# Kernel optimization log

Measured on AMD Instinct MI355X. Metric: run time of the kernel, lower is better.

The kernel has to match this reference:

```python
import jax, jax.numpy as jnp
from jax import lax
import numpy as np

B, T, U, V = 4, 300, 64, 1024
FEAT, H, L = 80, 512, 3            # encoder: 3-layer bidirectional LSTM
HD = 512                           # decoder hidden (1 layer)
ENC_OUT = DEC_OUT = 512
INNER = 512
DMAX = max(FEAT, 2 * H)            # padded input dim for stacked encoder weights
NEG = -1e30


def setup_inputs() -> dict:
    key = jax.random.key(0)
    ks = jax.random.split(key, 20)
    s = 1.0 / np.sqrt(H)
    u = lambda k, shp: jax.random.uniform(k, shp, jnp.float32, -s, s)
    inputs = jax.random.normal(ks[0], (B, T, FEAT), jnp.float32)
    inputs_length = jax.random.randint(ks[1], (B,), T // 2, T + 1, jnp.int32)
    targets = jax.random.randint(ks[2], (B, U), 1, V, jnp.int32)
    targets_length = jax.random.randint(ks[3], (B,), U // 2, U + 1, jnp.int32)
    enc_Wih = u(ks[4], (L, 2, 4 * H, DMAX))   # layer0 uses first FEAT cols
    enc_Whh = u(ks[5], (L, 2, 4 * H, H))
    enc_b = u(ks[6], (L, 2, 4 * H))           # b_ih + b_hh fused
    enc_proj_W = u(ks[7], (ENC_OUT, 2 * H))
    enc_proj_b = u(ks[8], (ENC_OUT,))
    dec_emb = u(ks[9], (V, HD)).at[0].set(0.0)  # padding_idx=0
    dec_Wih = u(ks[10], (4 * HD, HD))
    dec_Whh = u(ks[11], (4 * HD, HD))
    dec_b = u(ks[12], (4 * HD,))
    dec_proj_W = u(ks[13], (DEC_OUT, HD))
    dec_proj_b = u(ks[14], (DEC_OUT,))
    j_fwd_W = u(ks[15], (INNER, ENC_OUT + DEC_OUT))
    j_fwd_b = u(ks[16], (INNER,))
    j_proj_W = u(ks[17], (V, INNER))
    j_proj_b = u(ks[18], (V,))
    return dict(inputs=inputs, inputs_length=inputs_length, targets=targets,
                targets_length=targets_length, enc_Wih=enc_Wih, enc_Whh=enc_Whh,
                enc_b=enc_b, enc_proj_W=enc_proj_W, enc_proj_b=enc_proj_b,
                dec_emb=dec_emb, dec_Wih=dec_Wih, dec_Whh=dec_Whh, dec_b=dec_b,
                dec_proj_W=dec_proj_W, dec_proj_b=dec_proj_b, j_fwd_W=j_fwd_W,
                j_fwd_b=j_fwd_b, j_proj_W=j_proj_W, j_proj_b=j_proj_b)


def lstm_layer(x, Wih, Whh, b):
    # x: [B, T, Din]; torch gate order (i, f, g, o)
    Bb = x.shape[0]
    Hh = Whh.shape[1]
    xg = jnp.einsum('btd,gd->btg', x, Wih) + b  # precompute input projections

    def step(carry, xt):
        h, c = carry
        g = xt + h @ Whh.T
        i, f, gg, o = jnp.split(g, 4, axis=-1)
        c = jax.nn.sigmoid(f) * c + jax.nn.sigmoid(i) * jnp.tanh(gg)
        h = jax.nn.sigmoid(o) * jnp.tanh(c)
        return (h, c), h

    z = jnp.zeros((Bb, Hh), x.dtype)
    _, hs = lax.scan(step, (z, z), xg.transpose(1, 0, 2))
    return hs.transpose(1, 0, 2)


def reverse_padded(x, lengths):
    # reverse each sequence within its valid length (packed-sequence semantics)
    t = jnp.arange(x.shape[1])
    idx = jnp.where(t[None] < lengths[:, None], lengths[:, None] - 1 - t[None], t[None])
    return jnp.take_along_axis(x, idx[:, :, None], axis=1)


def rnnt_loss(log_probs, targets, T_len, U_len):
    # log_probs: [B, T, U+1, V], blank = 0
    Bb, Tt, U1, _ = log_probs.shape
    Uu = U1 - 1
    blank = log_probs[..., 0]                                   # [B,T,U+1]
    idx = jnp.broadcast_to(targets[:, None, :, None], (Bb, Tt, Uu, 1))
    lab = jnp.take_along_axis(log_probs[:, :, :Uu, :], idx, axis=3)[..., 0]  # [B,T,U]

    def row_update(a, c):
        # solves x[u] = logaddexp(a[u], x[u-1] + c[u-1]) via log-space cumsum
        C = jnp.concatenate([jnp.zeros((Bb, 1), a.dtype), jnp.cumsum(c, axis=1)], axis=1)
        return C + lax.cumlogsumexp(a - C, axis=1)

    a0 = jnp.full((Bb, U1), NEG, log_probs.dtype).at[:, 0].set(0.0)
    alpha0 = row_update(a0, lab[:, 0])

    def step(alpha_prev, xs):
        bl_prev, lab_t = xs
        alpha = row_update(alpha_prev + bl_prev, lab_t)
        return alpha, alpha

    xs = (blank[:, :-1].transpose(1, 0, 2), lab[:, 1:].transpose(1, 0, 2))
    _, alphas = lax.scan(step, alpha0, xs)                      # [T-1,B,U+1]
    alphas = jnp.concatenate([alpha0[None], alphas], axis=0)    # [T,B,U+1]
    b_idx = jnp.arange(Bb)
    ll = alphas[T_len - 1, b_idx, U_len] + blank[b_idx, T_len - 1, U_len]
    return -jnp.mean(ll)


def reference(inputs, inputs_length, targets, targets_length, enc_Wih, enc_Whh,
              enc_b, enc_proj_W, enc_proj_b, dec_emb, dec_Wih, dec_Whh, dec_b,
              dec_proj_W, dec_proj_b, j_fwd_W, j_fwd_b, j_proj_W, j_proj_b):
    # ---- encoder: stacked bi-LSTM + projection ----
    mask = (jnp.arange(T)[None] < inputs_length[:, None])[..., None].astype(inputs.dtype)
    x = inputs
    for l in range(L):
        Din = x.shape[-1]
        fwd = lstm_layer(x, enc_Wih[l, 0, :, :Din], enc_Whh[l, 0], enc_b[l, 0])
        bwd = reverse_padded(
            lstm_layer(reverse_padded(x, inputs_length), enc_Wih[l, 1, :, :Din],
                       enc_Whh[l, 1], enc_b[l, 1]), inputs_length)
        x = jnp.concatenate([fwd, bwd], axis=-1) * mask
    enc = jnp.einsum('bth,oh->bto', x, enc_proj_W) + enc_proj_b  # [B,T,ENC_OUT]

    # ---- decoder: blank-prepended targets -> embed -> LSTM -> projection ----
    dec_in = jnp.pad(targets, ((0, 0), (1, 0)))                  # [B,U+1]
    demb = dec_emb[dec_in]
    dmask = (jnp.arange(U + 1)[None] < (targets_length + 1)[:, None])[..., None].astype(demb.dtype)
    dh = lstm_layer(demb, dec_Wih, dec_Whh, dec_b) * dmask
    dec = jnp.einsum('buh,oh->buo', dh, dec_proj_W) + dec_proj_b  # [B,U+1,DEC_OUT]

    # ---- joint: broadcast T x (U+1), split concat-matmul into two matmuls ----
    We, Wd = j_fwd_W[:, :ENC_OUT], j_fwd_W[:, ENC_OUT:]
    hj = jnp.tanh(jnp.einsum('bto,io->bti', enc, We)[:, :, None, :]
                  + jnp.einsum('buo,io->bui', dec, Wd)[:, None, :, :] + j_fwd_b)
    logits = jnp.einsum('btui,vi->btuv', hj, j_proj_W) + j_proj_b  # [B,T,U+1,V]
    log_probs = jax.nn.log_softmax(logits, axis=-1)

    return rnnt_loss(log_probs, targets, inputs_length, targets_length)
```

## Files before the change

kernel.cpp:

```cpp
#include <hip/hip_runtime.h>
#include <hip/hip_bf16.h>

#define B_ 4
#define T_ 300
#define U_ 64
#define U1_ 65
#define V_ 1024
#define H_ 512
#define G4_ 2048
#define NW_ 32
#define RPB_ (T_ * U1_)
#define NTILE_ 305
#define RPAD_ 19520

typedef __hip_bfloat16 bf16;
typedef unsigned long long u64;
typedef __attribute__((ext_vector_type(8))) short short8;
typedef __attribute__((ext_vector_type(4))) float floatx4;

__device__ __forceinline__ float b2f(bf16 x) { return __bfloat162float(x); }
__device__ __forceinline__ bf16 f2b(float x) { return __float2bfloat16(x); }
__device__ __forceinline__ short bf16bits(float x) {
  bf16 h = __float2bfloat16(x);
  return *reinterpret_cast<short*>(&h);
}
__device__ __forceinline__ short8 pack8(float4 a, float4 b) {
  short8 p;
  p[0] = bf16bits(a.x); p[1] = bf16bits(a.y); p[2] = bf16bits(a.z); p[3] = bf16bits(a.w);
  p[4] = bf16bits(b.x); p[5] = bf16bits(b.y); p[6] = bf16bits(b.z); p[7] = bf16bits(b.w);
  return p;
}
__device__ __forceinline__ float sigm_(float x) { return 1.f / (1.f + __expf(-x)); }
__device__ __forceinline__ float tanh_(float x) { return 1.f - 2.f / (1.f + __expf(2.f * x)); }
__device__ __forceinline__ float lae_(float x, float y) {
  float m = fmaxf(x, y);
  float n = fminf(x, y);
  return m + __logf(1.f + __expf(n - m));
}

__global__ void zero_hpk_kernel(u64* __restrict__ a) {
  int i = blockIdx.x * 256 + threadIdx.x;
  if (i < 7 * 4096) a[i] = 0ull;
}

__global__ void prep_kernel(const float* __restrict__ in, bf16* __restrict__ x0) {
  int i = blockIdx.x * 256 + threadIdx.x;
  if (i < B_ * T_ * 128) {
    int k = i & 127;
    int row = i >> 7;
    float v = (k < 80) ? in[row * 80 + k] : 0.f;
    x0[(size_t)row * 1024 + k] = f2b(v);
  }
}

__global__ void embed_kernel(const float* __restrict__ emb, const int* __restrict__ tgt,
                             bf16* __restrict__ demb) {
  int i = blockIdx.x * 256 + threadIdx.x;
  if (i >= B_ * U1_ * 512) return;
  int k = i & 511;
  int bu = i >> 9;
  int u = bu % U1_, b = bu / U1_;
  int id = (u == 0) ? 0 : tgt[b * U_ + u - 1];
  demb[i] = f2b(emb[(size_t)id * 512 + k]);
}

__global__ __launch_bounds__(256) void gemm_kernel(
    const bf16* __restrict__ A, int lda,
    const float* __restrict__ W, int ldw,
    const float* __restrict__ bias,
    void* __restrict__ Cout, int out_f32, int ldc,
    int M, int K) {
  __shared__ __align__(16) bf16 As[64][72];
  __shared__ __align__(16) bf16 Bs[64][72];
  int m0 = blockIdx.x * 64, n0 = blockIdx.y * 64;
  int tid = threadIdx.x, w = tid >> 6, l = tid & 63;
  int l4 = l & 15, lq = l >> 4;
  floatx4 acc[4];
#pragma unroll
  for (int nt = 0; nt < 4; ++nt) acc[nt] = (floatx4){0.f, 0.f, 0.f, 0.f};
  for (int k0 = 0; k0 < K; k0 += 64) {
    __syncthreads();
#pragma unroll
    for (int q = 0; q < 2; ++q) {
      int cc = tid + q * 256;
      int r = cc >> 3, kc = (cc & 7) * 8;
      short8 va = {0, 0, 0, 0, 0, 0, 0, 0};
      int gm = m0 + r;
      if (gm < M) va = *(const short8*)(A + (size_t)gm * lda + k0 + kc);
      *(short8*)(&As[r][kc]) = va;
      const float* wp = W + (size_t)(n0 + r) * ldw + k0 + kc;
      float4 w0 = *(const float4*)(wp);
      float4 w1 = *(const float4*)(wp + 4);
      *(short8*)(&Bs[r][kc]) = pack8(w0, w1);
    }
    __syncthreads();
#pragma unroll
    for (int kk = 0; kk < 64; kk += 32) {
      short8 a = *(const short8*)(&As[w * 16 + l4][kk + lq * 8]);
#pragma unroll
      for (int nt = 0; nt < 4; ++nt) {
        short8 bb = *(const short8*)(&Bs[nt * 16 + l4][kk + lq * 8]);
        acc[nt] = __builtin_amdgcn_mfma_f32_16x16x32_bf16(a, bb, acc[nt], 0, 0, 0);
      }
    }
  }
#pragma unroll
  for (int nt = 0; nt < 4; ++nt) {
    int col = n0 + nt * 16 + l4;
    float bv = bias ? bias[col] : 0.f;
#pragma unroll
    for (int r = 0; r < 4; ++r) {
      int row = m0 + w * 16 + lq * 4 + r;
      if (row < M) {
        float v = acc[nt][r] + bv;
        if (out_f32) ((float*)Cout)[(size_t)row * ldc + col] = v;
        else ((bf16*)Cout)[(size_t)row * ldc + col] = f2b(v);
      }
    }
  }
}

__global__ __launch_bounds__(256, 1) void scan_kernel(
    const float* __restrict__ xg,
    const float* __restrict__ whh,
    const int* __restrict__ len_raw, int len_add,
    int Tmax, int bwd_mask,
    bf16* __restrict__ out, int out_stride,
    int dec_d,
    const float* __restrict__ xg2, const float* __restrict__ whh2,
    const int* __restrict__ len_raw2, int len_add2,
    int Tmax2, bf16* __restrict__ out2, int out_stride2,
    u64* __restrict__ hpk) {
  int w = blockIdx.x, d = blockIdx.y;
  int tid = threadIdx.x;
  bool isdec = (d == dec_d);
  const float* xg_d = isdec ? xg2 : xg + (size_t)d * B_ * Tmax * G4_;
  const float* whh_d = isdec ? whh2 : whh + (size_t)d * G4_ * H_;
  const int* lens = isdec ? len_raw2 : len_raw;
  int ladd = isdec ? len_add2 : len_add;
  int tmax = isdec ? Tmax2 : Tmax;
  bf16* outp = isdec ? out2 : out;
  int ostride = isdec ? out_stride2 : out_stride;
  int ocol = isdec ? 0 : d * H_;
  bool bwd = isdec ? false : ((bwd_mask >> d) & 1);
  u64* hp = hpk + (size_t)d * 4096;

  int sub = tid >> 6;
  int l = tid & 63;
  int col = l & 15;
  int lq = l >> 4;
  int gate = col & 3;
  int dloc = col >> 2;
  int dim = w * 16 + sub * 4 + dloc;
  int grow = gate * H_ + dim;
  int sb = l & 12;

  __shared__ int len_s[4];
  __shared__ __align__(16) bf16 h_lds[2][16][512];

  if (tid < 4) len_s[tid] = lens[tid] + ladd;
  {
    unsigned* hz = (unsigned*)&h_lds[0][0][0];
#pragma unroll
    for (int i = 0; i < 32; ++i) hz[tid + i * 256] = 0u;
  }

  short8 bfr[16];
  {
    const float* wp = whh_d + (size_t)grow * H_ + lq * 8;
#pragma unroll
    for (int ks2 = 0; ks2 < 16; ++ks2) {
      float4 w0 = *(const float4*)(wp + ks2 * 32);
      float4 w1 = *(const float4*)(wp + ks2 * 32 + 4);
      bfr[ks2] = pack8(w0, w1);
    }
  }
  __syncthreads();
  int smax = max(max(len_s[0], len_s[1]), max(len_s[2], len_s[3]));

  int D0 = sub * 128 + 2 * l;
  float cst = 0.f;
  char* hbase = (char*)&h_lds[0][0][0];
  unsigned rsw = (unsigned)((l & 7) << 4);
  unsigned rbyte = (unsigned)((l & 15) * 1024 + lq * 16);

  float xv[4];
  if (l < 16) {
#pragma unroll
    for (int b = 0; b < 4; ++b) {
      int lb = len_s[b];
      int rt = bwd ? (lb - 1) : 0;
      xv[b] = xg_d[((size_t)b * tmax + rt) * G4_ + grow];
    }
  }

  for (int s = 0; s < smax; ++s) {
    int p = s & 1;
    char* pl = hbase + p * 16384;
    if (s == 0) {
    } else {
      const u64* src = hp + ((s - 1) & 1) * 2048;
      u64 v[8];
      for (;;) {
        bool ok = true;
#pragma unroll
        for (int b = 0; b < 4; ++b) {
          v[2 * b] = __hip_atomic_load(src + b * 512 + D0, __ATOMIC_RELAXED,
                                       __HIP_MEMORY_SCOPE_AGENT);
          v[2 * b + 1] = __hip_atomic_load(src + b * 512 + D0 + 1, __ATOMIC_RELAXED,
                                           __HIP_MEMORY_SCOPE_AGENT);
          ok &= ((int)(unsigned)v[2 * b] == s) & ((int)(unsigned)v[2 * b + 1] == s);
        }
        if (__all(ok)) break;
      }
      unsigned cb = (unsigned)(D0 * 2);
#pragma unroll
      for (int b = 0; b < 4; ++b) {
        float f0 = __uint_as_float((unsigned)(v[2 * b] >> 32));
        float f1 = __uint_as_float((unsigned)(v[2 * b + 1] >> 32));
        bf16 h0 = f2b(f0), h1 = f2b(f1);
        float r0 = f0 - b2f(h0), r1 = f1 - b2f(h1);
        bf16 e0 = f2b(r0), e1 = f2b(r1);
        unsigned hi = (unsigned)*(unsigned short*)&h0 |
                      ((unsigned)*(unsigned short*)&h1 << 16);
        unsigned lo = (unsigned)*(unsigned short*)&e0 |
                      ((unsigned)*(unsigned short*)&e1 << 16);
        *(unsigned*)(pl + (((unsigned)(b * 1024) + cb) ^ (unsigned)(b << 4))) = hi;
        *(unsigned*)(pl + (((unsigned)((b + 4) * 1024) + cb) ^ (unsigned)((b + 4) << 4))) = lo;
      }
    }
    __syncthreads();
    float xvn[4];
    if (l < 16) {
      int sn = s + 1;
#pragma unroll
      for (int b = 0; b < 4; ++b) {
        int lb = len_s[b];
        int rt = bwd ? (lb - 1 - sn) : sn;
        if (sn >= lb) rt = 0;
        xvn[b] = xg_d[((size_t)b * tmax + rt) * G4_ + grow];
      }
    }
    floatx4 accA = (floatx4){0.f, 0.f, 0.f, 0.f};
    floatx4 accB = (floatx4){0.f, 0.f, 0.f, 0.f};
#pragma unroll
    for (int k2 = 0; k2 < 16; k2 += 2) {
      short8 a0 = *(const short8*)(pl + ((rbyte + (unsigned)(k2 * 64)) ^ rsw));
      short8 a1 = *(const short8*)(pl + ((rbyte + (unsigned)((k2 + 1) * 64)) ^ rsw));
      accA = __builtin_amdgcn_mfma_f32_16x16x32_bf16(a0, bfr[k2], accA, 0, 0, 0);
      accB = __builtin_amdgcn_mfma_f32_16x16x32_bf16(a1, bfr[k2 + 1], accB, 0, 0, 0);
    }
    floatx4 acc = accA + accB;
    float hout = 0.f;
#pragma unroll
    for (int r = 0; r < 4; ++r) {
      float v2 = acc[r] + __shfl(acc[r], col + 16, 64);
      if (l < 16) v2 += xv[r];
      float gi = __shfl(v2, sb + 0, 64);
      float gf = __shfl(v2, sb + 1, 64);
      float gg = __shfl(v2, sb + 2, 64);
      float go = __shfl(v2, sb + 3, 64);
      if (l < 16 && (l & 3) == r && s < len_s[r]) {
        cst = sigm_(gf) * cst + sigm_(gi) * tanh_(gg);
        hout = sigm_(go) * tanh_(cst);
      }
    }
    if (l < 16) {
      int b = l & 3;
      u64 pkt = ((u64)__float_as_uint(hout) << 32) | (unsigned)(s + 1);
      __hip_atomic_store(hp + p * 2048 + b * 512 + dim, pkt,
                         __ATOMIC_RELAXED, __HIP_MEMORY_SCOPE_AGENT);
      if (s < len_s[b]) {
        int t = bwd ? (len_s[b] - 1 - s) : s;
        outp[((size_t)b * tmax + t) * ostride + ocol + dim] = f2b(hout);
      }
    }
#pragma unroll
    for (int b = 0; b < 4; ++b) xv[b] = xvn[b];
  }
}

__global__ __launch_bounds__(256) void joint_kernel(
    const float* __restrict__ ea, const float* __restrict__ da,
    const float* __restrict__ Wp, const float* __restrict__ pb,
    const int* __restrict__ targets,
    float* __restrict__ blankraw, float* __restrict__ labraw,
    float* __restrict__ jstats) {
  __shared__ __align__(16) bf16 As[64][72];
  __shared__ __align__(16) bf16 Bs[256][72];
  __shared__ float bias_s[256];
  __shared__ int tgt_s[64];
  __shared__ float pstat[64][2][2];

  int tid = threadIdx.x;
  int tile = blockIdx.x, cb = blockIdx.y, b = blockIdx.z;
  int r0 = tile * 64;

  bias_s[tid & 255] = pb[cb * 256 + (tid & 255)];
  if (tid < 64) {
    int r = r0 + tid;
    int u = r % U1_;
    tgt_s[tid] = (r < RPB_ && u < U_) ? targets[b * U_ + u] : -1;
  }
  int si = tid >> 2;
  int sseg = (tid & 3) * 16;
  int sr = r0 + si;
  bool svalid = sr < RPB_;
  int st = svalid ? sr / U1_ : 0;
  int su = svalid ? sr % U1_ : 0;
  const float* ep = ea + ((size_t)(b * T_ + st)) * 512 + sseg;
  const float* dp = da + ((size_t)(b * U1_ + su)) * 512 + sseg;

  int wid = tid >> 6, l = tid & 63;
  int wm = wid >> 1, wn = wid & 1;
  int l4 = l & 15, lq = l >> 4;

  floatx4 acc[2][8];
#pragma unroll
  for (int ms = 0; ms < 2; ++ms)
#pragma unroll
    for (int nt = 0; nt < 8; ++nt) acc[ms][nt] = (floatx4){0.f, 0.f, 0.f, 0.f};

  for (int k0 = 0; k0 < 512; k0 += 64) {
    __syncthreads();
    {
      const float* e = ep + k0;
      const float* d = dp + k0;
#pragma unroll
      for (int h = 0; h < 2; ++h) {
        float4 e0 = *(const float4*)(e + h * 8);
        float4 e1 = *(const float4*)(e + h * 8 + 4);
        float4 d0 = *(const float4*)(d + h * 8);
        float4 d1 = *(const float4*)(d + h * 8 + 4);
        short8 pk = {0, 0, 0, 0, 0, 0, 0, 0};
        if (svalid) {
          pk[0] = bf16bits(tanh_(e0.x + d0.x));
          pk[1] = bf16bits(tanh_(e0.y + d0.y));
          pk[2] = bf16bits(tanh_(e0.z + d0.z));
          pk[3] = bf16bits(tanh_(e0.w + d0.w));
          pk[4] = bf16bits(tanh_(e1.x + d1.x));
          pk[5] = bf16bits(tanh_(e1.y + d1.y));
          pk[6] = bf16bits(tanh_(e1.z + d1.z));
          pk[7] = bf16bits(tanh_(e1.w + d1.w));
        }
        *(short8*)(&As[si][sseg + h * 8]) = pk;
      }
    }
#pragma unroll
    for (int q = 0; q < 8; ++q) {
      int cc = tid + q * 256;
      int r = cc >> 3, kc = (cc & 7) * 8;
      const float* wp = Wp + (size_t)(cb * 256 + r) * 512 + k0 + kc;
      float4 w0 = *(const float4*)(wp);
      float4 w1 = *(const float4*)(wp + 4);
      *(short8*)(&Bs[r][kc]) = pack8(w0, w1);
    }
    __syncthreads();
#pragma unroll
    for (int kk = 0; kk < 64; kk += 32) {
      short8 af[2], bf8[8];
#pragma unroll
      for (int ms = 0; ms < 2; ++ms)
        af[ms] = *(const short8*)(&As[wm * 32 + ms * 16 + l4][kk + lq * 8]);
#pragma unroll
      for (int nt = 0; nt < 8; ++nt)
        bf8[nt] = *(const short8*)(&Bs[wn * 128 + nt * 16 + l4][kk + lq * 8]);
#pragma unroll
      for (int ms = 0; ms < 2; ++ms)
#pragma unroll
        for (int nt = 0; nt < 8; ++nt)
          acc[ms][nt] = __builtin_amdgcn_mfma_f32_16x16x32_bf16(af[ms], bf8[nt], acc[ms][nt], 0, 0, 0);
    }
  }
#pragma unroll
  for (int ms = 0; ms < 2; ++ms) {
#pragma unroll
    for (int r = 0; r < 4; ++r) {
      int i = wm * 32 + ms * 16 + lq * 4 + r;
      int grow = r0 + i;
      bool valid = grow < RPB_;
      int tg = tgt_s[i];
      float v[8];
      float mx = -1e30f;
#pragma unroll
      for (int nt = 0; nt < 8; ++nt) {
        int colc = wn * 128 + nt * 16 + l4;
        float x = acc[ms][nt][r] + bias_s[colc];
        v[nt] = x;
        mx = fmaxf(mx, x);
        int gcol = cb * 256 + colc;
        if (valid) {
          if (gcol == 0) blankraw[(size_t)b * RPB_ + grow] = x;
          if (gcol == tg) labraw[(size_t)b * RPB_ + grow] = x;
        }
      }
#pragma unroll
      for (int dd = 1; dd < 16; dd <<= 1) mx = fmaxf(mx, __shfl_xor(mx, dd, 64));
      float se = 0.f;
#pragma unroll
      for (int nt = 0; nt < 8; ++nt) se += __expf(v[nt] - mx);
#pragma unroll
      for (int dd = 1; dd < 16; dd <<= 1) se += __shfl_xor(se, dd, 64);
      if (l4 == 0) { pstat[i][wn][0] = mx; pstat[i][wn][1] = se; }
    }
  }
  __syncthreads();
  if (tid < 64) {
    float ma = pstat[tid][0][0], sa = pstat[tid][0][1];
    float mb = pstat[tid][1][0], sb = pstat[tid][1][1];
    float mc = fmaxf(ma, mb);
    float sc = sa * __expf(ma - mc) + sb * __expf(mb - mc);
    size_t o = (((size_t)b * RPAD_ + r0 + tid) * 4 + cb) * 2;
    jstats[o] = mc;
    jstats[o + 1] = sc;
  }
}

__global__ void finalize_kernel(const float* __restrict__ jstats,
                                float* __restrict__ blank, float* __restrict__ lab) {
  int g = blockIdx.x * 256 + threadIdx.x;
  if (g >= B_ * RPB_) return;
  int b = g / RPB_, r = g % RPB_;
  const float* st = jstats + ((size_t)b * RPAD_ + r) * 8;
  float M = fmaxf(fmaxf(st[0], st[2]), fmaxf(st[4], st[6]));
  float s = st[1] * __expf(st[0] - M) + st[3] * __expf(st[2] - M) +
            st[5] * __expf(st[4] - M) + st[7] * __expf(st[6] - M);
  float lse = M + __logf(s);
  blank[g] -= lse;
  if ((r % U1_) < U_) lab[g] -= lse;
}

__global__ void loss_kernel(const float* __restrict__ blank, const float* __restrict__ lab,
                            const int* __restrict__ Tl, const int* __restrict__ Ul,
                            float* __restrict__ outp) {
  int b = threadIdx.x >> 6;
  int l = threadIdx.x & 63;
  int TL = Tl[b], UL = Ul[b];
  float alpha_l = 0.f, alpha0 = 0.f;
  for (int t = 0; t < TL; ++t) {
    float a_u0, a_l1;
    if (t == 0) { a_u0 = 0.f; a_l1 = -1e30f; }
    else {
      const float* bl = blank + ((size_t)b * T_ + (t - 1)) * U1_;
      a_u0 = alpha0 + bl[0];
      a_l1 = alpha_l + bl[l + 1];
    }
    const float* lb = lab + ((size_t)b * T_ + t) * U1_;
    float C = lb[l];
#pragma unroll
    for (int dd = 1; dd < 64; dd <<= 1) {
      float o = __shfl_up(C, dd, 64);
      if (l >= dd) C += o;
    }
    float S = a_l1 - C;
#pragma unroll
    for (int dd = 1; dd < 64; dd <<= 1) {
      float o = __shfl_up(S, dd, 64);
      if (l >= dd) S = lae_(S, o);
    }
    alpha_l = C + lae_(a_u0, S);
    alpha0 = a_u0;
  }
  float av = (UL == 0) ? alpha0 : __shfl(alpha_l, UL - 1, 64);
  float ll = av + blank[((size_t)b * T_ + (TL - 1)) * U1_ + UL];
  __shared__ float lls[4];
  if (l == 0) lls[b] = ll;
  __syncthreads();
  if (threadIdx.x == 0) outp[0] = -0.25f * (lls[0] + lls[1] + lls[2] + lls[3]);
}

static constexpr size_t OFF_XG = 0;
static constexpr size_t OFF_XA = OFF_XG + (size_t)2 * B_ * T_ * G4_ * 4;
static constexpr size_t OFF_XB = OFF_XA + (size_t)B_ * T_ * 1024 * 2;
static constexpr size_t OFF_ENC = OFF_XB + (size_t)B_ * T_ * 1024 * 2;
static constexpr size_t OFF_EA = OFF_ENC + (size_t)B_ * T_ * 512 * 2;
static constexpr size_t OFF_DEMB = OFF_EA + (size_t)B_ * T_ * 512 * 4;
static constexpr size_t OFF_DXG = OFF_DEMB + (size_t)B_ * U1_ * 512 * 2;
static constexpr size_t OFF_DH = OFF_DXG + (size_t)B_ * U1_ * G4_ * 4;
static constexpr size_t OFF_DEC = OFF_DH + (size_t)B_ * U1_ * 512 * 2;
static constexpr size_t OFF_DA = OFF_DEC + (size_t)B_ * U1_ * 512 * 2;
static constexpr size_t OFF_BL = OFF_DA + (size_t)B_ * U1_ * 512 * 4;
static constexpr size_t OFF_LAB = OFF_BL + (size_t)B_ * T_ * U1_ * 4;
static constexpr size_t OFF_HPK = OFF_LAB + (size_t)B_ * T_ * U1_ * 4;
static constexpr size_t OFF_JST = OFF_HPK + (size_t)7 * 4096 * 8;

extern "C" void kernel_launch(void* const* d_in, const int* in_sizes, int n_in,
                              void* d_out, int out_size, void* d_ws, size_t ws_size,
                              hipStream_t stream) {
  (void)in_sizes; (void)n_in; (void)out_size; (void)ws_size;
  const float* inputs = (const float*)d_in[0];
  const int* inputs_length = (const int*)d_in[1];
  const int* targets = (const int*)d_in[2];
  const int* targets_length = (const int*)d_in[3];
  const float* enc_Wih = (const float*)d_in[4];
  const float* enc_Whh = (const float*)d_in[5];
  const float* enc_b = (const float*)d_in[6];
  const float* enc_proj_W = (const float*)d_in[7];
  const float* enc_proj_b = (const float*)d_in[8];
  const float* dec_emb = (const float*)d_in[9];
  const float* dec_Wih = (const float*)d_in[10];
  const float* dec_Whh = (const float*)d_in[11];
  const float* dec_b = (const float*)d_in[12];
  const float* dec_proj_W = (const float*)d_in[13];
  const float* dec_proj_b = (const float*)d_in[14];
  const float* j_fwd_W = (const float*)d_in[15];
  const float* j_fwd_b = (const float*)d_in[16];
  const float* j_proj_W = (const float*)d_in[17];
  const float* j_proj_b = (const float*)d_in[18];

  char* ws = (char*)d_ws;
  float* xg = (float*)(ws + OFF_XG);
  bf16* xa = (bf16*)(ws + OFF_XA);
  bf16* xb = (bf16*)(ws + OFF_XB);
  bf16* encb = (bf16*)(ws + OFF_ENC);
  float* eab = (float*)(ws + OFF_EA);
  bf16* demb = (bf16*)(ws + OFF_DEMB);
  float* dxg = (float*)(ws + OFF_DXG);
  bf16* dh = (bf16*)(ws + OFF_DH);
  bf16* decb = (bf16*)(ws + OFF_DEC);
  float* dab = (float*)(ws + OFF_DA);
  float* blank = (float*)(ws + OFF_BL);
  float* lab = (float*)(ws + OFF_LAB);
  u64* hpk = (u64*)(ws + OFF_HPK);
  float* jstats = (float*)(ws + OFF_JST);

  zero_hpk_kernel<<<112, 256, 0, stream>>>(hpk);
  prep_kernel<<<600, 256, 0, stream>>>(inputs, xa);
  embed_kernel<<<520, 256, 0, stream>>>(dec_emb, targets, demb);

  gemm_kernel<<<dim3(5, 32), 256, 0, stream>>>(demb, 512, dec_Wih, 512, dec_b,
                                               dxg, 1, G4_, B_ * U1_, 512);
  for (int dd = 0; dd < 2; ++dd) {
    gemm_kernel<<<dim3(19, 32), 256, 0, stream>>>(
        xa, 1024, enc_Wih + (size_t)dd * G4_ * 1024, 1024, enc_b + (size_t)dd * G4_,
        xg + (size_t)dd * B_ * T_ * G4_, 1, G4_, B_ * T_, 128);
  }
  scan_kernel<<<dim3(NW_, 3), 256, 0, stream>>>(
      xg, enc_Whh, inputs_length, 0, T_, 2, xb, 1024,
      2, dxg, dec_Whh, targets_length, 1, U1_, dh, 512,
      hpk);

  gemm_kernel<<<dim3(5, 8), 256, 0, stream>>>(dh, 512, dec_proj_W, 512, dec_proj_b,
                                              decb, 0, 512, B_ * U1_, 512);
  gemm_kernel<<<dim3(5, 8), 256, 0, stream>>>(decb, 512, j_fwd_W + 512, 1024, j_fwd_b,
                                              dab, 1, 512, B_ * U1_, 512);

  bf16* xcur = xb;
  for (int lyr = 1; lyr < 3; ++lyr) {
    bf16* xnext = (xcur == xa) ? xb : xa;
    for (int dd = 0; dd < 2; ++dd) {
      gemm_kernel<<<dim3(19, 32), 256, 0, stream>>>(
          xcur, 1024,
          enc_Wih + (size_t)(lyr * 2 + dd) * G4_ * 1024, 1024,
          enc_b + (size_t)(lyr * 2 + dd) * G4_,
          xg + (size_t)dd * B_ * T_ * G4_, 1, G4_, B_ * T_, 1024);
    }
    scan_kernel<<<dim3(NW_, 2), 256, 0, stream>>>(
        xg, enc_Whh + (size_t)lyr * 2 * G4_ * H_,
        inputs_length, 0, T_, 2, xnext, 1024,
        -1, dxg, dec_Whh, targets_length, 1, U1_, dh, 512,
        hpk + (size_t)(3 + 2 * (lyr - 1)) * 4096);
    xcur = xnext;
  }
  gemm_kernel<<<dim3(19, 8), 256, 0, stream>>>(xcur, 1024, enc_proj_W, 1024, enc_proj_b,
                                               encb, 0, 512, B_ * T_, 1024);
  gemm_kernel<<<dim3(19, 8), 256, 0, stream>>>(encb, 512, j_fwd_W, 1024, (const float*)nullptr,
                                               eab, 1, 512, B_ * T_, 512);

  joint_kernel<<<dim3(NTILE_, 4, B_), 256, 0, stream>>>(eab, dab, j_proj_W, j_proj_b, targets,
                                                        blank, lab, jstats);
  finalize_kernel<<<(B_ * RPB_ + 255) / 256, 256, 0, stream>>>(jstats, blank, lab);
  loss_kernel<<<1, 256, 0, stream>>>(blank, lab, inputs_length, targets_length, (float*)d_out);
}
```

Baseline: 3.361 ms.

## Compute joint tanh activations once per row tile and pre-pack projection weights to bf16

The joint kernel now builds the full 64x512 tanh(enc+dec) activation tile in LDS once and loops over the four 256-column vocab chunks inside one block, instead of launching a separate block per chunk that recomputed the activations. A new pre-pass converts the joint projection weights to bf16 once, so the inner loop copies bf16 directly instead of converting fp32 on every load. The trade-off is a 4x smaller grid (1220 blocks), much larger LDS per block (about 66KB+), and serialized chunk work per block, which may reduce occupancy and parallelism.

```diff
diff --git a/kernel.cpp b/kernel.cpp
--- a/kernel.cpp
+++ b/kernel.cpp
@@ -41,6 +41,11 @@
 __global__ void zero_hpk_kernel(u64* __restrict__ a) {
   int i = blockIdx.x * 256 + threadIdx.x;
   if (i < 7 * 4096) a[i] = 0ull;
+}
+
+__global__ void packw_kernel(const float* __restrict__ W, bf16* __restrict__ Wb, int n) {
+  int i = blockIdx.x * 256 + threadIdx.x;
+  if (i < n) Wb[i] = f2b(W[i]);
 }
 
 __global__ void prep_kernel(const float* __restrict__ in, bf16* __restrict__ x0) {
@@ -197,8 +202,7 @@
   for (int s = 0; s < smax; ++s) {
     int p = s & 1;
     char* pl = hbase + p * 16384;
-    if (s == 0) {
-    } else {
+    if (s > 0) {
       const u64* src = hp + ((s - 1) & 1) * 2048;
       u64 v[8];
       for (;;) {
@@ -282,21 +286,20 @@
 
 __global__ __launch_bounds__(256) void joint_kernel(
     const float* __restrict__ ea, const float* __restrict__ da,
-    const float* __restrict__ Wp, const float* __restrict__ pb,
+    const bf16* __restrict__ Wpb, const float* __restrict__ pb,
     const int* __restrict__ targets,
     float* __restrict__ blankraw, float* __restrict__ labraw,
     float* __restrict__ jstats) {
-  __shared__ __align__(16) bf16 As[64][72];
+  __shared__ __align__(16) bf16 As[64][520];
   __shared__ __align__(16) bf16 Bs[256][72];
   __shared__ float bias_s[256];
   __shared__ int tgt_s[64];
   __shared__ float pstat[64][2][2];
 
   int tid = threadIdx.x;
-  int tile = blockIdx.x, cb = blockIdx.y, b = blockIdx.z;
+  int tile = blockIdx.x, b = blockIdx.y;
   int r0 = tile * 64;
 
-  bias_s[tid & 255] = pb[cb * 256 + (tid & 255)];
   if (tid < 64) {
     int r = r0 + tid;
     int u = r % U1_;
@@ -311,108 +314,112 @@
   const float* ep = ea + ((size_t)(b * T_ + st)) * 512 + sseg;
   const float* dp = da + ((size_t)(b * U1_ + su)) * 512 + sseg;
 
+#pragma unroll
+  for (int k0s = 0; k0s < 512; k0s += 64) {
+    const float* e = ep + k0s;
+    const float* d = dp + k0s;
+#pragma unroll
+    for (int h = 0; h < 2; ++h) {
+      float4 e0 = *(const float4*)(e + h * 8);
+      float4 e1 = *(const float4*)(e + h * 8 + 4);
+      float4 d0 = *(const float4*)(d + h * 8);
+      float4 d1 = *(const float4*)(d + h * 8 + 4);
+      short8 pk = {0, 0, 0, 0, 0, 0, 0, 0};
+      if (svalid) {
+        pk[0] = bf16bits(tanh_(e0.x + d0.x));
+        pk[1] = bf16bits(tanh_(e0.y + d0.y));
+        pk[2] = bf16bits(tanh_(e0.z + d0.z));
+        pk[3] = bf16bits(tanh_(e0.w + d0.w));
+        pk[4] = bf16bits(tanh_(e1.x + d1.x));
+        pk[5] = bf16bits(tanh_(e1.y + d1.y));
+        pk[6] = bf16bits(tanh_(e1.z + d1.z));
+        pk[7] = bf16bits(tanh_(e1.w + d1.w));
+      }
+      *(short8*)(&As[si][k0s + sseg + h * 8]) = pk;
+    }
+  }
+
   int wid = tid >> 6, l = tid & 63;
   int wm = wid >> 1, wn = wid & 1;
   int l4 = l & 15, lq = l >> 4;
 
-  floatx4 acc[2][8];
-#pragma unroll
-  for (int ms = 0; ms < 2; ++ms)
-#pragma unroll
-    for (int nt = 0; nt < 8; ++nt) acc[ms][nt] = (floatx4){0.f, 0.f, 0.f, 0.f};
-
-  for (int k0 = 0; k0 < 512; k0 += 64) {
+  for (int cb = 0; cb < 4; ++cb) {
+    bias_s[tid] = pb[cb * 256 + tid];
+
+    floatx4 acc[2][8];
+#pragma unroll
+    for (int ms = 0; ms < 2; ++ms)
+#pragma unroll
+      for (int nt = 0; nt < 8; ++nt) acc[ms][nt] = (floatx4){0.f, 0.f, 0.f, 0.f};
+
+    for (int k0 = 0; k0 < 512; k0 += 64) {
+      __syncthreads();
+#pragma unroll
+      for (int q = 0; q < 8; ++q) {
+        int cc = tid + q * 256;
+        int r = cc >> 3, kc = (cc & 7) * 8;
+        *(short8*)(&Bs[r][kc]) =
+            *(const short8*)(Wpb + (size_t)(cb * 256 + r) * 512 + k0 + kc);
+      }
+      __syncthreads();
+#pragma unroll
+      for (int kk = 0; kk < 64; kk += 32) {
+        short8 af[2], bf8[8];
+#pragma unroll
+        for (int ms = 0; ms < 2; ++ms)
+          af[ms] = *(const short8*)(&As[wm * 32 + ms * 16 + l4][k0 + kk + lq * 8]);
+#pragma unroll
+        for (int nt = 0; nt < 8; ++nt)
+          bf8[nt] = *(const short8*)(&Bs[wn * 128 + nt * 16 + l4][kk + lq * 8]);
+#pragma unroll
+        for (int ms = 0; ms < 2; ++ms)
+#pragma unroll
+          for (int nt = 0; nt < 8; ++nt)
+            acc[ms][nt] = __builtin_amdgcn_mfma_f32_16x16x32_bf16(af[ms], bf8[nt], acc[ms][nt], 0, 0, 0);
+      }
+    }
+#pragma unroll
+    for (int ms = 0; ms < 2; ++ms) {
+#pragma unroll
+      for (int r = 0; r < 4; ++r) {
+        int i = wm * 32 + ms * 16 + lq * 4 + r;
+        int grow = r0 + i;
+        bool valid = grow < RPB_;
+        int tg = tgt_s[i];
+        float v[8];
+        float mx = -1e30f;
+#pragma unroll
+        for (int nt = 0; nt < 8; ++nt) {
+          int colc = wn * 128 + nt * 16 + l4;
+          float x = acc[ms][nt][r] + bias_s[colc];
+          v[nt] = x;
+          mx = fmaxf(mx, x);
+          int gcol = cb * 256 + colc;
+          if (valid) {
+            if (gcol == 0) blankraw[(size_t)b * RPB_ + grow] = x;
+            if (gcol == tg) labraw[(size_t)b * RPB_ + grow] = x;
+          }
+        }
+#pragma unroll
+        for (int dd = 1; dd < 16; dd <<= 1) mx = fmaxf(mx, __shfl_xor(mx, dd, 64));
+        float se = 0.f;
+#pragma unroll
+        for (int nt = 0; nt < 8; ++nt) se += __expf(v[nt] - mx);
+#pragma unroll
+        for (int dd = 1; dd < 16; dd <<= 1) se += __shfl_xor(se, dd, 64);
+        if (l4 == 0) { pstat[i][wn][0] = mx; pstat[i][wn][1] = se; }
+      }
+    }
     __syncthreads();
-    {
-      const float* e = ep + k0;
-      const float* d = dp + k0;
-#pragma unroll
-      for (int h = 0; h < 2; ++h) {
-        float4 e0 = *(const float4*)(e + h * 8);
-        float4 e1 = *(const float4*)(e + h * 8 + 4);
-        float4 d0 = *(const float4*)(d + h * 8);
-        float4 d1 = *(const float4*)(d + h * 8 + 4);
-        short8 pk = {0, 0, 0, 0, 0, 0, 0, 0};
-        if (svalid) {
-          pk[0] = bf16bits(tanh_(e0.x + d0.x));
-          pk[1] = bf16bits(tanh_(e0.y + d0.y));
-          pk[2] = bf16bits(tanh_(e0.z + d0.z));
-          pk[3] = bf16bits(tanh_(e0.w + d0.w));
-          pk[4] = bf16bits(tanh_(e1.x + d1.x));
-          pk[5] = bf16bits(tanh_(e1.y + d1.y));
-          pk[6] = bf16bits(tanh_(e1.z + d1.z));
-          pk[7] = bf16bits(tanh_(e1.w + d1.w));
-        }
-        *(short8*)(&As[si][sseg + h * 8]) = pk;
-      }
-    }
-#pragma unroll
-    for (int q = 0; q < 8; ++q) {
-      int cc = tid + q * 256;
-      int r = cc >> 3, kc = (cc & 7) * 8;
-      const float* wp = Wp + (size_t)(cb * 256 + r) * 512 + k0 + kc;
-      float4 w0 = *(const float4*)(wp);
-      float4 w1 = *(const float4*)(wp + 4);
-      *(short8*)(&Bs[r][kc]) = pack8(w0, w1);
-    }
-    __syncthreads();
-#pragma unroll
-    for (int kk = 0; kk < 64; kk += 32) {
-      short8 af[2], bf8[8];
-#pragma unroll
-      for (int ms = 0; ms < 2; ++ms)
-        af[ms] = *(const short8*)(&As[wm * 32 + ms * 16 + l4][kk + lq * 8]);
-#pragma unroll
-      for (int nt = 0; nt < 8; ++nt)
-        bf8[nt] = *(const short8*)(&Bs[wn * 128 + nt * 16 + l4][kk + lq * 8]);
-#pragma unroll
-      for (int ms = 0; ms < 2; ++ms)
-#pragma unroll
-        for (int nt = 0; nt < 8; ++nt)
-          acc[ms][nt] = __builtin_amdgcn_mfma_f32_16x16x32_bf16(af[ms], bf8[nt], acc[ms][nt], 0, 0, 0);
-    }
-  }
-#pragma unroll
-  for (int ms = 0; ms < 2; ++ms) {
-#pragma unroll
-    for (int r = 0; r < 4; ++r) {
-      int i = wm * 32 + ms * 16 + lq * 4 + r;
-      int grow = r0 + i;
-      bool valid = grow < RPB_;
-      int tg = tgt_s[i];
-      float v[8];
-      float mx = -1e30f;
-#pragma unroll
-      for (int nt = 0; nt < 8; ++nt) {
-        int colc = wn * 128 + nt * 16 + l4;
-        float x = acc[ms][nt][r] + bias_s[colc];
-        v[nt] = x;
-        mx = fmaxf(mx, x);
-        int gcol = cb * 256 + colc;
-        if (valid) {
-          if (gcol == 0) blankraw[(size_t)b * RPB_ + grow] = x;
-          if (gcol == tg) labraw[(size_t)b * RPB_ + grow] = x;
-        }
-      }
-#pragma unroll
-      for (int dd = 1; dd < 16; dd <<= 1) mx = fmaxf(mx, __shfl_xor(mx, dd, 64));
-      float se = 0.f;
-#pragma unroll
-      for (int nt = 0; nt < 8; ++nt) se += __expf(v[nt] - mx);
-#pragma unroll
-      for (int dd = 1; dd < 16; dd <<= 1) se += __shfl_xor(se, dd, 64);
-      if (l4 == 0) { pstat[i][wn][0] = mx; pstat[i][wn][1] = se; }
-    }
-  }
-  __syncthreads();
-  if (tid < 64) {
-    float ma = pstat[tid][0][0], sa = pstat[tid][0][1];
-    float mb = pstat[tid][1][0], sb = pstat[tid][1][1];
-    float mc = fmaxf(ma, mb);
-    float sc = sa * __expf(ma - mc) + sb * __expf(mb - mc);
-    size_t o = (((size_t)b * RPAD_ + r0 + tid) * 4 + cb) * 2;
-    jstats[o] = mc;
-    jstats[o + 1] = sc;
+    if (tid < 64) {
+      float ma = pstat[tid][0][0], sa = pstat[tid][0][1];
+      float mb = pstat[tid][1][0], sb = pstat[tid][1][1];
+      float mc = fmaxf(ma, mb);
+      float sc = sa * __expf(ma - mc) + sb * __expf(mb - mc);
+      size_t o = (((size_t)b * RPAD_ + r0 + tid) * 4 + cb) * 2;
+      jstats[o] = mc;
+      jstats[o + 1] = sc;
+    }
   }
 }
 
@@ -483,6 +490,7 @@
 static constexpr size_t OFF_LAB = OFF_BL + (size_t)B_ * T_ * U1_ * 4;
 static constexpr size_t OFF_HPK = OFF_LAB + (size_t)B_ * T_ * U1_ * 4;
 static constexpr size_t OFF_JST = OFF_HPK + (size_t)7 * 4096 * 8;
+static constexpr size_t OFF_WPB = OFF_JST + (size_t)B_ * RPAD_ * 4 * 2 * 4;
 
 extern "C" void kernel_launch(void* const* d_in, const int* in_sizes, int n_in,
                               void* d_out, int out_size, void* d_ws, size_t ws_size,
@@ -523,8 +531,10 @@
   float* lab = (float*)(ws + OFF_LAB);
   u64* hpk = (u64*)(ws + OFF_HPK);
   float* jstats = (float*)(ws + OFF_JST);
+  bf16* wpb = (bf16*)(ws + OFF_WPB);
 
   zero_hpk_kernel<<<112, 256, 0, stream>>>(hpk);
+  packw_kernel<<<2048, 256, 0, stream>>>(j_proj_W, wpb, V_ * 512);
   prep_kernel<<<600, 256, 0, stream>>>(inputs, xa);
   embed_kernel<<<520, 256, 0, stream>>>(dec_emb, targets, demb);
 
@@ -567,8 +577,8 @@
   gemm_kernel<<<dim3(19, 8), 256, 0, stream>>>(encb, 512, j_fwd_W, 1024, (const float*)nullptr,
                                                eab, 1, 512, B_ * T_, 512);
 
-  joint_kernel<<<dim3(NTILE_, 4, B_), 256, 0, stream>>>(eab, dab, j_proj_W, j_proj_b, targets,
-                                                        blank, lab, jstats);
+  joint_kernel<<<dim3(NTILE_, B_), 256, 0, stream>>>(eab, dab, wpb, j_proj_b, targets,
+                                                     blank, lab, jstats);
   finalize_kernel<<<(B_ * RPB_ + 255) / 256, 256, 0, stream>>>(jstats, blank, lab);
   loss_kernel<<<1, 256, 0, stream>>>(blank, lab, inputs_length, targets_length, (float*)d_out);
 }
```

Result: no change. 3.336 ms (-0.7%).
